# Performance work log

Hardware: AMD Instinct MI355X
Metric: run time of the kernel (lower is better)

The kernel has to match this reference:

```python
import jax, jax.numpy as jnp
import numpy as np

H_IMG = W_IMG = 1024
H_MAP = W_MAP = 64
SCALE = 16  # img // fmap, both axes
SCALES = [2, 2.5, 3, 3.5, 4, 5]
RATIOS = [0.5, 1.5, 2.0, 2.5, 3, 3.5, 4]
A = len(SCALES) * len(RATIOS)  # 42
POS_T, NEG_T = 0.5, 0.3


def _anchors_np():
    # generate_base_anchors + generate_anchor_boxes (down_h = down_w = SCALE)
    base = np.zeros((A, 4), np.float32)
    cy = cx = SCALE / 2.0
    i = 0
    for s in SCALES:
        for ar in RATIOS:
            h = SCALE * s * np.sqrt(ar)
            w = SCALE * s * np.sqrt(1.0 / ar)
            base[i] = [cy - h / 2.0, cx - w / 2.0, cy + h / 2.0, cx + w / 2.0]
            i += 1
    sy = np.arange(H_MAP) * SCALE
    sx = np.arange(W_MAP) * SCALE
    gx, gy = np.meshgrid(sx, sy)
    shifts = np.stack([gy.ravel(), gx.ravel(), gy.ravel(), gx.ravel()], axis=1)
    # order (H, W, A) -> matches conf.permute(0,2,3,1) flatten
    return (base[None, :, :] + shifts[:, None, :]).reshape(-1, 4).astype(np.float32)


def _conv(x, w, b):
    y = jax.lax.conv_general_dilated(x, w, (1, 1), 'SAME',
                                     dimension_numbers=('NCHW', 'OIHW', 'NCHW'))
    return y + b[None, :, None, None]


def setup_inputs() -> dict:
    key = jax.random.key(0)
    ks = jax.random.split(key, 10)
    B, N, C, Hm, Wm, HID = 8, 20, 256, 64, 64, 512
    feature_map = jax.random.normal(ks[0], (B, C, Hm, Wm), dtype=jnp.float32)
    # valid GT boxes in pixel xyxy-style (d0<d2, d1<d3), last 5 per image padded -1
    p0 = jax.random.uniform(ks[1], (B, N)) * 860.0
    p1 = jax.random.uniform(ks[2], (B, N)) * 860.0
    s0 = jax.random.uniform(ks[3], (B, N)) * 144.0 + 16.0
    s1 = jax.random.uniform(ks[4], (B, N)) * 144.0 + 16.0
    gt_bboxes = jnp.stack([p0, p1, p0 + s0, p1 + s1], axis=-1)
    gt_bboxes = gt_bboxes.at[:, 15:, :].set(-1.0)
    gt_classes = jax.random.randint(ks[5], (B, N), 0, 10)
    conv1_w = jax.random.normal(ks[6], (HID, C, 3, 3), dtype=jnp.float32) * 0.02
    conv1_b = jnp.zeros((HID,), jnp.float32)
    conf_w = jax.random.normal(ks[7], (A, HID, 1, 1), dtype=jnp.float32) * 0.02
    conf_b = jnp.zeros((A,), jnp.float32)
    reg_w = jax.random.normal(ks[8], (4 * A, HID, 1, 1), dtype=jnp.float32) * 0.02
    reg_b = jnp.zeros((4 * A,), jnp.float32)
    return {"feature_map": feature_map, "gt_bboxes": gt_bboxes, "gt_classes": gt_classes,
            "conv1_w": conv1_w, "conv1_b": conv1_b, "conf_w": conf_w, "conf_b": conf_b,
            "reg_w": reg_w, "reg_b": reg_b}


def reference(feature_map, gt_bboxes, gt_classes, conv1_w, conv1_b,
              conf_w, conf_b, reg_w, reg_b):
    anc = jnp.asarray(_anchors_np())           # [M,4]
    B = feature_map.shape[0]
    M = anc.shape[0]                           # H*W*A

    # project_bboxes p2a: divide by scale, keep -1 padding
    pad = gt_bboxes == -1.0
    g = jnp.where(pad, -1.0, gt_bboxes / float(SCALE))  # [B,N,4]
    valid = g[..., 0] >= 0                                # [B,N]
    g_safe = jnp.where(valid[..., None], g, jnp.array([0.0, 0.0, 1.0, 1.0]))

    # pairwise IoU [B,M,N] (vectorized get_iou_mat; invalid GT -> 0)
    tl = jnp.maximum(anc[None, :, None, :2], g_safe[:, None, :, :2])
    br = jnp.minimum(anc[None, :, None, 2:], g_safe[:, None, :, 2:])
    wh = jnp.clip(br - tl, 0.0)
    inter = wh[..., 0] * wh[..., 1]
    area_a = (anc[:, 2] - anc[:, 0]) * (anc[:, 3] - anc[:, 1])
    area_g = (g_safe[..., 2] - g_safe[..., 0]) * (g_safe[..., 3] - g_safe[..., 1])
    iou = inter / (area_a[None, :, None] + area_g[:, None, :] - inter)
    iou = jnp.where(valid[:, None, :], iou, 0.0)

    # positive assignment: per-GT argmax anchors + IoU > pos_thresh
    max_per_gt = iou.max(axis=1, keepdims=True)            # [B,1,N]
    pos_mask = ((iou == max_per_gt) & (max_per_gt > 0)) | (iou > POS_T)
    pos_any = pos_mask.any(axis=-1)                        # [B,M]
    a2g = jnp.argmax(iou, axis=2)                          # [B,M]
    max_per_anc = iou.max(axis=2)                          # [B,M]

    gt_for_anc = jnp.take_along_axis(g_safe, a2g[:, :, None], axis=1)  # [B,M,4]
    anc_b = jnp.broadcast_to(anc, (B, M, 4))
    gt_sel = jnp.where(pos_any[..., None], gt_for_anc, anc_b)  # safe for log

    # calc_gt_offsets (cxcywh encode), computed for all anchors, masked later
    a_c = (anc_b[..., :2] + anc_b[..., 2:]) * 0.5
    a_s = anc_b[..., 2:] - anc_b[..., :2]
    g_c = (gt_sel[..., :2] + gt_sel[..., 2:]) * 0.5
    g_s = gt_sel[..., 2:] - gt_sel[..., :2]
    off_gt = jnp.concatenate([(g_c - a_c) / a_s, jnp.log(g_s / a_s)], axis=-1)
    off_gt = off_gt.reshape(-1, 4)                          # [B*M,4]

    # ProposalModule head (dropout is a no-op in eval)
    x = jax.nn.relu(_conv(feature_map, conv1_w, conv1_b))
    conf = _conv(x, conf_w, conf_b)                         # [B,A,H,W]
    reg = _conv(x, reg_w, reg_b)                            # [B,4A,H,W]
    cflat = conf.transpose(0, 2, 3, 1).reshape(-1)          # [B*M]
    offp = reg.transpose(0, 2, 3, 1).reshape(-1, 4)         # [B*M,4]

    pf = pos_any.reshape(-1).astype(jnp.float32)
    P = pf.sum()

    # cls loss: BCE-with-logits, label 1 on positives, 0 on P sampled negatives
    cls_pos = (jax.nn.softplus(-cflat) * pf).sum() / P
    neg = max_per_anc.reshape(-1) < NEG_T
    scores = jax.random.uniform(jax.random.key(7), cflat.shape)
    scores = jnp.where(neg, scores, 2.0)
    ranks = jnp.argsort(jnp.argsort(scores))               # random sample = rank < P
    sel = (neg & (ranks < P)).astype(jnp.float32)
    cls_neg = (jax.nn.softplus(cflat) * sel).sum() / sel.sum()
    cls_loss = 0.5 * (cls_pos + cls_neg)

    d = offp - off_gt
    ad = jnp.abs(d)
    sl1 = jnp.where(ad < 1.0, 0.5 * ad * ad, ad - 0.5)
    reg_loss = (sl1 * pf[:, None]).sum() / (P * 4.0)

    return cls_loss + reg_loss
```

## Files before the change

kernel.cpp:

```cpp
#include <hip/hip_runtime.h>
#include <hip/hip_fp16.h>
#include <stdint.h>

constexpr int B_  = 8, HM = 64, WM = 64, A_ = 42, CIN = 256, HIDN = 512;
constexpr int M_  = HM * WM * A_;
constexpr int NA  = B_ * M_;
constexpr int HALF = NA / 2;
constexpr int KK  = CIN * 9;
constexpr float POS_T = 0.5f;

constexpr int WINY = 10, WINX = 10, WPIX = WINY * WINX;
constexpr int PERIMG = A_ * WPIX;
constexpr int WBLK = (PERIMG + 511) / 512;
constexpr int NMAXB = WBLK * B_;

constexpr int MAXPOS = 4096, MAXSEL = 4096;
constexpr int MAXPIX = 1024;
constexpr uint32_t VCAND = 16384u;
constexpr int NBIN = 128, CAP = 96;

constexpr int KCH = 288;

constexpr int NWIN = NMAXB;
constexpr int NRND = 168;
constexpr int NWCV = 72;
constexpr int NBLK_TF = NWIN + NRND + NWCV;

constexpr size_t OFF_CTRL  = 0;
constexpr size_t OFF_MAXGT = 256;
constexpr size_t OFF_BINSP = 1024;
constexpr size_t OFF_SLOT  = 9216;
constexpr size_t MS_END    = 140288;
constexpr size_t OFF_PLIST = 140288;
constexpr size_t OFF_POSL  = 144384;
constexpr size_t OFF_SELL  = 160768;
constexpr size_t OFF_CAND  = 177152;
constexpr size_t OFF_APATCH= 8689664;
constexpr size_t OFF_WF16  = 13408256;
constexpr size_t OFF_HFIN  = 15767552;


__device__ __forceinline__ unsigned short f2bf(float f) {
  uint32_t x = __float_as_uint(f);
  uint32_t r = x + 0x7FFFu + ((x >> 16) & 1u);
  return (unsigned short)(r >> 16);
}
__device__ __forceinline__ float bf2f(unsigned short h) {
  return __uint_as_float(((uint32_t)h) << 16);
}
__device__ __forceinline__ uint32_t f2h2(float a, float b) {
  return (uint32_t)__half_as_ushort(__float2half_rn(a)) |
         ((uint32_t)__half_as_ushort(__float2half_rn(b)) << 16);
}

typedef _Float16 h8v __attribute__((ext_vector_type(8)));
typedef float f4v __attribute__((ext_vector_type(4)));

__device__ __forceinline__ float iou_pair(float ay0, float ax0, float ay1, float ax1,
                                          float areaA, float g0, float g1, float g2, float g3,
                                          float areaG) {
#pragma clang fp contract(off)
  float ty = fmaxf(ay0, g0), tx = fmaxf(ax0, g1);
  float by = fminf(ay1, g2), bx = fminf(ax1, g3);
  float hy = by - ty; hy = fmaxf(hy, 0.f);
  float hx = bx - tx; hx = fmaxf(hx, 0.f);
  float inter = hy * hx;
  return inter / (areaA + areaG - inter);
}

__device__ __forceinline__ void anchor_box(const float* basef, int a, int y, int x,
                                           float& ay0, float& ax0, float& ay1, float& ax1,
                                           float& areaA) {
#pragma clang fp contract(off)
  double sy = 16.0 * (double)y, sx = 16.0 * (double)x;
  ay0 = (float)((double)basef[a * 4 + 0] + sy);
  ax0 = (float)((double)basef[a * 4 + 1] + sx);
  ay1 = (float)((double)basef[a * 4 + 2] + sy);
  ax1 = (float)((double)basef[a * 4 + 3] + sx);
  areaA = (ay1 - ay0) * (ax1 - ax0);
}

__device__ __forceinline__ void fill_base(float* sbase, int t) {
  if (t < 42) {
    const double SC[6] = {2.0, 2.5, 3.0, 3.5, 4.0, 5.0};
    const double RA[7] = {0.5, 1.5, 2.0, 2.5, 3.0, 3.5, 4.0};
    int si = t / 7, ri = t - si * 7;
    double h = 16.0 * SC[si] * sqrt(RA[ri]);
    double w = 16.0 * SC[si] * sqrt(1.0 / RA[ri]);
    sbase[t * 4 + 0] = (float)(8.0 - h / 2.0);
    sbase[t * 4 + 1] = (float)(8.0 - w / 2.0);
    sbase[t * 4 + 2] = (float)(8.0 + h / 2.0);
    sbase[t * 4 + 3] = (float)(8.0 + w / 2.0);
  }
}

__device__ __forceinline__ void fill_gt(const float* gt, int b, float* sg, float* sarea,
                                        unsigned* sval, int t) {
  if (t < 20) {
#pragma clang fp contract(off)
    float g4[4];
    for (int d = 0; d < 4; d++) {
      float v = gt[(b * 20 + t) * 4 + d];
      g4[d] = (v == -1.0f) ? -1.0f : v * 0.0625f;
    }
    unsigned valid = (g4[0] >= 0.0f) ? 1u : 0u;
    if (!valid) { g4[0] = 0.f; g4[1] = 0.f; g4[2] = 1.f; g4[3] = 1.f; }
    sg[t * 4 + 0] = g4[0]; sg[t * 4 + 1] = g4[1]; sg[t * 4 + 2] = g4[2]; sg[t * 4 + 3] = g4[3];
    sarea[t] = (g4[2] - g4[0]) * (g4[3] - g4[1]);
    sval[t] = valid;
  }
}

__device__ __forceinline__ void claim_pixel(char* ws, int pixg) {
  int* slotmap = (int*)(ws + OFF_SLOT);
  if (atomicCAS((unsigned*)&slotmap[pixg], 0u, 0xFFFFFFFFu) == 0u) {
    unsigned s = atomicAdd((unsigned*)(ws + OFF_CTRL) + 2, 1u);
    if (s < MAXPIX) { ((int*)(ws + OFF_PLIST))[s] = pixg; slotmap[pixg] = (int)s + 1; }
    else slotmap[pixg] = -1;
  }
}

__device__ __forceinline__ float softplusf(float x) {
  return fmaxf(x, 0.f) + log1pf(expf(-fabsf(x)));
}
__device__ __forceinline__ float sl1(float d) {
  float ad = fabsf(d);
  return ad < 1.f ? 0.5f * ad * ad : ad - 0.5f;
}

__device__ __forceinline__ void tf_round(uint32_t& x0, uint32_t& x1, int r) {
  x0 += x1; x1 = (x1 << r) | (x1 >> (32 - r)); x1 ^= x0;
}
__device__ __forceinline__ void threefry(uint32_t c0, uint32_t c1, uint32_t& o0, uint32_t& o1) {
  const uint32_t k0 = 0u, k1 = 7u;
  const uint32_t k2 = k0 ^ k1 ^ 0x1BD11BDAu;
  uint32_t x0 = c0 + k0, x1 = c1 + k1;
  tf_round(x0, x1, 13); tf_round(x0, x1, 15); tf_round(x0, x1, 26); tf_round(x0, x1, 6);
  x0 += k1; x1 += k2 + 1u;
  tf_round(x0, x1, 17); tf_round(x0, x1, 29); tf_round(x0, x1, 16); tf_round(x0, x1, 24);
  x0 += k2; x1 += k0 + 2u;
  tf_round(x0, x1, 13); tf_round(x0, x1, 15); tf_round(x0, x1, 26); tf_round(x0, x1, 6);
  x0 += k0; x1 += k1 + 3u;
  tf_round(x0, x1, 17); tf_round(x0, x1, 29); tf_round(x0, x1, 16); tf_round(x0, x1, 24);
  x0 += k1; x1 += k2 + 4u;
  tf_round(x0, x1, 13); tf_round(x0, x1, 15); tf_round(x0, x1, 26); tf_round(x0, x1, 6);
  x0 += k2; x1 += k0 + 5u;
  o0 = x0; o1 = x1;
}

__device__ __forceinline__ void emit_cand(char* ws, uint32_t v, uint32_t p) {
  if (v < VCAND) {
    unsigned bin = v >> 7;
    unsigned slot = atomicAdd((unsigned*)(ws + OFF_BINSP) + bin * 16, 1u);
    if (slot < (unsigned)CAP)
      ((uint2*)(ws + OFF_CAND))[bin * CAP + slot] = make_uint2(v, p);
  }
}

__global__ void __launch_bounds__(512) kTF(const float* __restrict__ gt,
                                           const float* __restrict__ w1, char* ws) {
  __shared__ float sbase[168], sg[80], sarea[20];
  __shared__ unsigned sval[20];
  __shared__ int smax[20];
  int t = threadIdx.x;
  if (blockIdx.x < NWIN) {
    int b = blockIdx.x / WBLK, blk = blockIdx.x - b * WBLK;
    fill_base(sbase, t);
    fill_gt(gt, b, sg, sarea, sval, t);
    if (t < 20) smax[t] = 0;
    __syncthreads();
    int idx = blk * 512 + t;
    bool ok = idx < PERIMG;
    float ay0 = 0.f, ax0 = 0.f, ay1 = 0.f, ax1 = 0.f, areaA = 1.f;
    if (ok) {
      int a = idx / WPIX, pp = idx - a * WPIX;
      int y = pp / WINX, x = pp - y * WINX;
      anchor_box(sbase, a, y, x, ay0, ax0, ay1, ax1, areaA);
    }
#pragma unroll
    for (int n = 0; n < 20; n++) {
      float io = 0.f;
      if (ok && sval[n]) io = iou_pair(ay0, ax0, ay1, ax1, areaA,
                                       sg[n * 4], sg[n * 4 + 1], sg[n * 4 + 2],
                                       sg[n * 4 + 3], sarea[n]);
#pragma unroll
      for (int off = 32; off >= 1; off >>= 1) io = fmaxf(io, __shfl_xor(io, off, 64));
      if ((t & 63) == 0 && io > 0.f) atomicMax(&smax[n], __float_as_int(io));
    }
    __syncthreads();
    if (t < 20 && smax[t] != 0)
      atomicMax((int*)(ws + OFF_MAXGT) + b * 20 + t, smax[t]);
  } else if (blockIdx.x < NWIN + NRND) {
    int p0 = ((int)blockIdx.x - NWIN) * 512 + t;
#pragma unroll
    for (int it = 0; it < 8; it++) {
      int p = p0 + it * (NRND * 512);
      uint32_t o0, o1; threefry((uint32_t)p, (uint32_t)(p + HALF), o0, o1);
      emit_cand(ws, o0 >> 9, (uint32_t)p);
      emit_cand(ws, o1 >> 9, (uint32_t)(p + HALF));
    }
  } else {
    int q0 = ((int)blockIdx.x - (NWIN + NRND)) * 512 + t;
#pragma unroll
    for (int it = 0; it < 8; it++) {
      int q = q0 + it * (NWCV * 512);
      float4 v = ((const float4*)w1)[q];
      uint2 o;
      o.x = f2h2(v.x, v.y);
      o.y = f2h2(v.z, v.w);
      ((uint2*)(ws + OFF_WF16))[q] = o;
    }
  }
}

__global__ void __launch_bounds__(512) kPos2(const float* __restrict__ gt, char* ws) {
  __shared__ float sbase[168], sg[80], sarea[20], smg[20];
  __shared__ unsigned sval[20];
  __shared__ unsigned scnt[128];
  __shared__ unsigned s_r, s_ucut;
  __shared__ int s_icut, s_cutbin, s_last;
  int b = blockIdx.y, t = threadIdx.x, lane = t & 63;
  unsigned* ctrl = (unsigned*)(ws + OFF_CTRL);
  fill_base(sbase, t);
  fill_gt(gt, b, sg, sarea, sval, t);
  if (t < 20) smg[t] = __int_as_float(((int*)(ws + OFF_MAXGT))[b * 20 + t]);
  __syncthreads();
  int idx = blockIdx.x * 512 + t;
  bool pos = false;
  unsigned packv = 0;
  int pixg = 0;
  if (idx < PERIMG) {
    int a = idx / WPIX, pp = idx - a * WPIX;
    int y = pp / WINX, x = pp - y * WINX;
    float ay0, ax0, ay1, ax1, areaA;
    anchor_box(sbase, a, y, x, ay0, ax0, ay1, ax1, areaA);
    float best = -1.f; int arg = 0;
#pragma unroll
    for (int n = 0; n < 20; n++) {
      float io = 0.f;
      if (sval[n]) io = iou_pair(ay0, ax0, ay1, ax1, areaA,
                                 sg[n * 4], sg[n * 4 + 1], sg[n * 4 + 2],
                                 sg[n * 4 + 3], sarea[n]);
      if (io > best) { best = io; arg = n; }
      float mg = smg[n];
      pos = pos || ((io == mg) && (mg > 0.f)) || (io > POS_T);
    }
    if (pos) {
      int pix = y * 64 + x;
      int i = b * M_ + pix * 42 + a;
      packv = (unsigned)i | ((unsigned)arg << 21);
      pixg = b * 4096 + pix;
    }
  }
  unsigned long long mask = __ballot(pos);
  if (mask) {
    int leader = (int)__ffsll(mask) - 1;
    unsigned base = 0;
    if (lane == leader) base = atomicAdd(&ctrl[0], (unsigned)__popcll(mask));
    base = (unsigned)__shfl((int)base, leader, 64);
    if (pos) {
      unsigned slot = base + (unsigned)__popcll(mask & ((1ull << lane) - 1ull));
      if (slot < MAXPOS) ((unsigned*)(ws + OFF_POSL))[slot] = packv;
      claim_pixel(ws, pixg);
    }
  }
  __syncthreads();
  if (t == 0) {
    unsigned r = __hip_atomic_fetch_add(&ctrl[11], 1u, __ATOMIC_RELAXED,
                                        __HIP_MEMORY_SCOPE_AGENT);
    s_last = (r == (unsigned)(WBLK * B_) - 1) ? 1 : 0;
  }
  __syncthreads();
  if (!s_last) return;
  const uint2* bucket = (const uint2*)(ws + OFF_CAND);
  unsigned P = min(__hip_atomic_load(&ctrl[0], __ATOMIC_RELAXED,
                                     __HIP_MEMORY_SCOPE_AGENT), (unsigned)MAXPOS);
  if (t < 128)
    scnt[t] = min(__hip_atomic_load((unsigned*)(ws + OFF_BINSP) + t * 16,
                                    __ATOMIC_RELAXED, __HIP_MEMORY_SCOPE_AGENT),
                  (unsigned)CAP);
  __syncthreads();
  if (t == 0) {
    unsigned cum = 0; int c = 0;
    for (; c < 128; c++) { if (cum + scnt[c] >= P) break; cum += scnt[c]; }
    if (c == 128) c = 127;
    s_cutbin = c; s_r = (P > cum) ? (P - cum) : 0u;
  }
  __syncthreads();
  int cutbin = s_cutbin;
  unsigned n = scnt[cutbin];
  unsigned r = s_r; if (r > n) r = n;
  if (r == 0) {
    if (t == 0) { s_ucut = 0; s_icut = -1; }
  } else if (t < (int)n) {
    uint2 mine = bucket[cutbin * CAP + t];
    unsigned rank = 0;
    for (unsigned j = 0; j < n; j++) {
      uint2 o = bucket[cutbin * CAP + j];
      if (o.x < mine.x || (o.x == mine.x && (int)o.y < (int)mine.y)) rank++;
    }
    if (rank == r - 1) { s_ucut = mine.x; s_icut = (int)mine.y; }
  }
  __syncthreads();
  unsigned ucut = s_ucut; int icut = s_icut;
  for (unsigned j = t; j < (unsigned)(NBIN * CAP); j += 512) {
    unsigned bin = j / CAP, k = j - bin * CAP;
    bool sel = false; uint2 cj = make_uint2(0u, 0u);
    if (k < scnt[bin]) {
      cj = bucket[j];
      sel = (cj.x < ucut) || (cj.x == ucut && (int)cj.y <= icut);
    }
    unsigned long long m2 = __ballot(sel);
    if (m2) {
      int leader = (int)__ffsll(m2) - 1;
      unsigned base = 0;
      if (lane == leader) base = atomicAdd(&ctrl[1], (unsigned)__popcll(m2));
      base = (unsigned)__shfl((int)base, leader, 64);
      if (sel) {
        unsigned slot = base + (unsigned)__popcll(m2 & ((1ull << lane) - 1ull));
        if (slot < MAXSEL) {
          ((int*)(ws + OFF_SELL))[slot] = (int)cj.y;
          int bb = (int)cj.y / M_; int m = (int)cj.y - bb * M_;
          claim_pixel(ws, bb * 4096 + m / 42);
        }
      }
    }
  }
}

__global__ void __launch_bounds__(256) kIm2col(const float* __restrict__ fm, char* ws) {
  unsigned* ctrl = (unsigned*)(ws + OFF_CTRL);
  int npix = min((int)ctrl[2], MAXPIX);
  int chunk = blockIdx.y;
  int u0 = chunk * 384;
  for (int blk = blockIdx.x; blk < npix; blk += gridDim.x) {
    int pixg = ((const int*)(ws + OFF_PLIST))[blk];
    int b = pixg >> 12, pix = pixg & 4095;
    int y = pix >> 6, x = pix & 63;
    uint32_t* Ap = (uint32_t*)(ws + OFF_APATCH) + (size_t)blk * (KK / 2);
    for (int u = u0 + threadIdx.x; u < u0 + 384; u += 256) {
      float v[2];
#pragma unroll
      for (int h = 0; h < 2; h++) {
        int k = 2 * u + h;
        int ic = k / 9, r = k - ic * 9;
        int dy = r / 3, dx = r - dy * 3;
        int yy = y + dy - 1, xx = x + dx - 1;
        float vv = 0.f;
        if (yy >= 0 && yy < 64 && xx >= 0 && xx < 64)
          vv = fm[(((size_t)b * CIN + ic) * 64 + yy) * 64 + xx];
        v[h] = vv;
      }
      Ap[u] = f2h2(v[0], v[1]);
    }
  }
}

__global__ void __launch_bounds__(512) kGemm(const float* __restrict__ b1, char* ws) {
  __shared__ float red[8][16][132];
  unsigned* ctrl = (unsigned*)(ws + OFF_CTRL);
  int npix = min((int)ctrl[2], MAXPIX);
  int strip = blockIdx.x, och = blockIdx.y;
  int px0 = strip * 16;
  if (px0 >= npix) return;
  int oc0 = och * 128;
  const _Float16* Ap = (const _Float16*)(ws + OFF_APATCH);
  const _Float16* Wf = (const _Float16*)(ws + OFF_WF16);
  int t = threadIdx.x, lane = t & 63, wv = t >> 6;
  int kq = lane >> 4;
  int kb = wv * KCH;
  const _Float16* Arow = Ap + (size_t)(px0 + (lane & 15)) * KK + kb + kq * 8;
  const _Float16* Wrow = Wf + (size_t)(oc0 + (lane & 15)) * KK + kb + kq * 8;
  f4v acc[8] = {};
#pragma unroll 3
  for (int s = 0; s < 9; s++) {
    h8v a = *(const h8v*)(Arow + s * 32);
#pragma unroll
    for (int o = 0; o < 8; o++) {
      h8v bfr = *(const h8v*)(Wrow + (size_t)o * 16 * KK + s * 32);
      acc[o] = __builtin_amdgcn_mfma_f32_16x16x32_f16(a, bfr, acc[o], 0, 0, 0);
    }
  }
#pragma unroll
  for (int o = 0; o < 8; o++) {
    int col = o * 16 + (lane & 15);
#pragma unroll
    for (int r = 0; r < 4; r++)
      red[wv][kq * 4 + r][col] = acc[o][r];
  }
  __syncthreads();
  int row = t >> 5, colg = t & 31;
  if (px0 + row < npix) {
    float s4[4];
#pragma unroll
    for (int j = 0; j < 4; j++) s4[j] = b1[oc0 + colg * 4 + j];
#pragma unroll
    for (int w = 0; w < 8; w++)
#pragma unroll
      for (int j = 0; j < 4; j++) s4[j] += red[w][row][colg * 4 + j];
#pragma unroll
    for (int j = 0; j < 4; j++) s4[j] = fmaxf(s4[j], 0.f);
    unsigned short* hf = (unsigned short*)(ws + OFF_HFIN);
    uint2 o2;
    o2.x = f2h2(s4[0], s4[1]);
    o2.y = f2h2(s4[2], s4[3]);
    *(uint2*)(hf + (size_t)(px0 + row) * HIDN + oc0 + colg * 4) = o2;
  }
}

__global__ void __launch_bounds__(256) kHead(const float* __restrict__ gt,
                                             const float* __restrict__ cw,
                                             const float* __restrict__ cb,
                                             const float* __restrict__ rw,
                                             const float* __restrict__ rb,
                                             char* ws, float* out) {
  __shared__ float sbase[168], sg[640];
  __shared__ float sacc[3];
  int t = threadIdx.x;
  fill_base(sbase, t);
  if (t < 160) {
#pragma clang fp contract(off)
    float g4[4];
    for (int d = 0; d < 4; d++) {
      float v = gt[t * 4 + d];
      g4[d] = (v == -1.0f) ? -1.0f : v * 0.0625f;
    }
    if (!(g4[0] >= 0.0f)) { g4[0] = 0.f; g4[1] = 0.f; g4[2] = 1.f; g4[3] = 1.f; }
    sg[t * 4 + 0] = g4[0]; sg[t * 4 + 1] = g4[1];
    sg[t * 4 + 2] = g4[2]; sg[t * 4 + 3] = g4[3];
  }
  if (t < 3) sacc[t] = 0.f;
  __syncthreads();
  unsigned* ctrl = (unsigned*)(ws + OFF_CTRL);
  float* accum = (float*)(ctrl + 16);
  int np = min((int)ctrl[0], MAXPOS);
  int ns = min((int)ctrl[1], MAXSEL);
  int nent = np + ns;
  const unsigned* posl = (const unsigned*)(ws + OFF_POSL);
  const int* sell = (const int*)(ws + OFF_SELL);
  const int* slotmap = (const int*)(ws + OFF_SLOT);
  const unsigned short* hfin = (const unsigned short*)(ws + OFF_HFIN);
  int lane = t & 63;
  int gwave = blockIdx.x * 4 + (t >> 6);
  int nwaves = gridDim.x * 4;
  for (int e = gwave; e < nent; e += nwaves) {
    bool isPos = e < np;
    int i, arg = 0;
    if (isPos) { unsigned pck = posl[e]; i = (int)(pck & 0x1FFFFFu); arg = (int)(pck >> 21); }
    else i = sell[e - np];
    int b = i / M_; int m = i - b * M_;
    int pix = m / 42; int a = m - pix * 42;
    int y = pix >> 6, x = pix & 63;
    int slot = slotmap[b * 4096 + pix] - 1;
    if (slot < 0 || slot >= MAXPIX) continue;
    float h[8];
    {
      h8v hv = *(const h8v*)(hfin + (size_t)slot * HIDN + lane * 8);
#pragma unroll
      for (int j = 0; j < 8; j++) h[j] = (float)hv[j];
    }
    const float* cwr = cw + (size_t)a * HIDN + lane * 8;
    float4 cA = *(const float4*)cwr;
    float4 cB = *(const float4*)(cwr + 4);
    float cp = h[0] * cA.x + h[1] * cA.y + h[2] * cA.z + h[3] * cA.w +
               h[4] * cB.x + h[5] * cB.y + h[6] * cB.z + h[7] * cB.w;
#pragma unroll
    for (int off = 32; off >= 1; off >>= 1) cp += __shfl_xor(cp, off, 64);
    float conf = cp + cb[a];
    if (isPos) {
      float rp[4];
#pragma unroll
      for (int d = 0; d < 4; d++) {
        const float* rwr = rw + (size_t)(a * 4 + d) * HIDN + lane * 8;
        float4 rA = *(const float4*)rwr;
        float4 rB = *(const float4*)(rwr + 4);
        float sd = h[0] * rA.x + h[1] * rA.y + h[2] * rA.z + h[3] * rA.w +
                   h[4] * rB.x + h[5] * rB.y + h[6] * rB.z + h[7] * rB.w;
#pragma unroll
        for (int off = 32; off >= 1; off >>= 1) sd += __shfl_xor(sd, off, 64);
        rp[d] = sd + rb[a * 4 + d];
      }
      if (lane == 0) {
#pragma clang fp contract(off)
        float ay0, ax0, ay1, ax1, areaA;
        anchor_box(sbase, a, y, x, ay0, ax0, ay1, ax1, areaA);
        const float* g = sg + (size_t)(b * 20 + arg) * 4;
        float acy = (ay0 + ay1) * 0.5f, acx = (ax0 + ax1) * 0.5f;
        float ah = ay1 - ay0, aw = ax1 - ax0;
        float gcy = (g[0] + g[2]) * 0.5f, gcx = (g[1] + g[3]) * 0.5f;
        float gh = g[2] - g[0], gw = g[3] - g[1];
        float t0 = (gcy - acy) / ah, t1 = (gcx - acx) / aw;
        float t2 = logf(gh / ah), t3 = logf(gw / aw);
        float sL = sl1(rp[0] - t0) + sl1(rp[1] - t1) + sl1(rp[2] - t2) + sl1(rp[3] - t3);
        atomicAdd(&sacc[2], sL);
        atomicAdd(&sacc[0], softplusf(-conf));
      }
    } else {
      if (lane == 0) atomicAdd(&sacc[1], softplusf(conf));
    }
  }
  __syncthreads();
  if (t == 0) {
    if (sacc[0] != 0.f) atomicAdd(&accum[0], sacc[0]);
    if (sacc[1] != 0.f) atomicAdd(&accum[1], sacc[1]);
    if (sacc[2] != 0.f) atomicAdd(&accum[2], sacc[2]);
    asm volatile("s_waitcnt vmcnt(0)" ::: "memory");
    unsigned done = __hip_atomic_fetch_add(&ctrl[10], 1u, __ATOMIC_RELAXED,
                                           __HIP_MEMORY_SCOPE_AGENT);
    if (done == gridDim.x - 1) {
      float a0 = __hip_atomic_load(&accum[0], __ATOMIC_RELAXED, __HIP_MEMORY_SCOPE_AGENT);
      float a1 = __hip_atomic_load(&accum[1], __ATOMIC_RELAXED, __HIP_MEMORY_SCOPE_AGENT);
      float a2 = __hip_atomic_load(&accum[2], __ATOMIC_RELAXED, __HIP_MEMORY_SCOPE_AGENT);
      float P = (float)min((int)ctrl[0], MAXPOS);
      float S = (float)min((int)ctrl[1], MAXSEL);
      float cls = 0.5f * (a0 / P + a1 / S);
      out[0] = cls + a2 / (P * 4.0f);
    }
  }
}

extern "C" void kernel_launch(void* const* d_in, const int* in_sizes, int n_in,
                              void* d_out, int out_size, void* d_ws, size_t ws_size,
                              hipStream_t stream) {
  const float* fm = (const float*)d_in[0];
  const float* gt = (const float*)d_in[1];
  const float* w1 = (const float*)d_in[3];
  const float* b1 = (const float*)d_in[4];
  const float* cw = (const float*)d_in[5];
  const float* cb = (const float*)d_in[6];
  const float* rw = (const float*)d_in[7];
  const float* rb = (const float*)d_in[8];
  char* ws = (char*)d_ws;
  float* out = (float*)d_out;

  hipMemsetAsync(ws, 0, MS_END, stream);
  kTF<<<NBLK_TF, 512, 0, stream>>>(gt, w1, ws);
  kPos2<<<dim3(WBLK, B_), 512, 0, stream>>>(gt, ws);
  kIm2col<<<dim3(128, 3), 256, 0, stream>>>(fm, ws);
  kGemm<<<dim3(MAXPIX / 16, 4), 512, 0, stream>>>(b1, ws);
  kHead<<<256, 256, 0, stream>>>(gt, cw, cb, rw, rb, ws, out);
}
```

Baseline: 162.6 us.

## Move weight fp16 cast into im2col launch and widen GEMM pixel tile

The conv1 weight fp32-to-fp16 conversion moves out of the first kernel and into extra blocks of the im2col launch, so it overlaps with patch gathering and stays off the early critical path. The GEMM now gives each block 32 pixels, with 2 pixel groups and 4 K chunks instead of 8 K chunks over 16 pixels. This halves the block count and reuses each loaded weight fragment across twice as many pixels, at the cost of a longer per-wave K loop. The head grid doubles to 512 blocks, and an atomic load of the bin counters becomes a plain load.

New measurement: 183.5 us. +12.8%, slower.

```diff
diff --git a/kernel.cpp b/kernel.cpp
--- a/kernel.cpp
+++ b/kernel.cpp
@@ -19,12 +19,13 @@
 constexpr uint32_t VCAND = 16384u;
 constexpr int NBIN = 128, CAP = 96;
 
-constexpr int KCH = 288;
-
 constexpr int NWIN = NMAXB;
 constexpr int NRND = 168;
-constexpr int NWCV = 72;
-constexpr int NBLK_TF = NWIN + NRND + NWCV;
+constexpr int NBLK_TF = NWIN + NRND;
+
+constexpr int NI2C = 128, NWCV = 72;
+
+constexpr int KCH4 = 576;
 
 constexpr size_t OFF_CTRL  = 0;
 constexpr size_t OFF_MAXGT = 256;
@@ -40,14 +41,6 @@
 constexpr size_t OFF_HFIN  = 15767552;
 
 
-__device__ __forceinline__ unsigned short f2bf(float f) {
-  uint32_t x = __float_as_uint(f);
-  uint32_t r = x + 0x7FFFu + ((x >> 16) & 1u);
-  return (unsigned short)(r >> 16);
-}
-__device__ __forceinline__ float bf2f(unsigned short h) {
-  return __uint_as_float(((uint32_t)h) << 16);
-}
 __device__ __forceinline__ uint32_t f2h2(float a, float b) {
   return (uint32_t)__half_as_ushort(__float2half_rn(a)) |
          ((uint32_t)__half_as_ushort(__float2half_rn(b)) << 16);
@@ -157,8 +150,7 @@
   }
 }
 
-__global__ void __launch_bounds__(512) kTF(const float* __restrict__ gt,
-                                           const float* __restrict__ w1, char* ws) {
+__global__ void __launch_bounds__(512) kTF(const float* __restrict__ gt, char* ws) {
   __shared__ float sbase[168], sg[80], sarea[20];
   __shared__ unsigned sval[20];
   __shared__ int smax[20];
@@ -190,7 +182,7 @@
     __syncthreads();
     if (t < 20 && smax[t] != 0)
       atomicMax((int*)(ws + OFF_MAXGT) + b * 20 + t, smax[t]);
-  } else if (blockIdx.x < NWIN + NRND) {
+  } else {
     int p0 = ((int)blockIdx.x - NWIN) * 512 + t;
 #pragma unroll
     for (int it = 0; it < 8; it++) {
@@ -198,17 +190,6 @@
       uint32_t o0, o1; threefry((uint32_t)p, (uint32_t)(p + HALF), o0, o1);
       emit_cand(ws, o0 >> 9, (uint32_t)p);
       emit_cand(ws, o1 >> 9, (uint32_t)(p + HALF));
-    }
-  } else {
-    int q0 = ((int)blockIdx.x - (NWIN + NRND)) * 512 + t;
-#pragma unroll
-    for (int it = 0; it < 8; it++) {
-      int q = q0 + it * (NWCV * 512);
-      float4 v = ((const float4*)w1)[q];
-      uint2 o;
-      o.x = f2h2(v.x, v.y);
-      o.y = f2h2(v.z, v.w);
-      ((uint2*)(ws + OFF_WF16))[q] = o;
     }
   }
 }
@@ -276,9 +257,7 @@
   unsigned P = min(__hip_atomic_load(&ctrl[0], __ATOMIC_RELAXED,
                                      __HIP_MEMORY_SCOPE_AGENT), (unsigned)MAXPOS);
   if (t < 128)
-    scnt[t] = min(__hip_atomic_load((unsigned*)(ws + OFF_BINSP) + t * 16,
-                                    __ATOMIC_RELAXED, __HIP_MEMORY_SCOPE_AGENT),
-                  (unsigned)CAP);
+    scnt[t] = min(((const unsigned*)(ws + OFF_BINSP))[t * 16], (unsigned)CAP);
   __syncthreads();
   if (t == 0) {
     unsigned cum = 0; int c = 0;
@@ -328,12 +307,27 @@
   }
 }
 
-__global__ void __launch_bounds__(256) kIm2col(const float* __restrict__ fm, char* ws) {
+__global__ void __launch_bounds__(256) kIm2col(const float* __restrict__ fm,
+                                               const float* __restrict__ w1, char* ws) {
+  if (blockIdx.x >= NI2C) {
+    if (blockIdx.y != 0) return;
+    int q0 = ((int)blockIdx.x - NI2C) * 256 + threadIdx.x;
+#pragma unroll
+    for (int it = 0; it < 16; it++) {
+      int q = q0 + it * (NWCV * 256);
+      float4 v = ((const float4*)w1)[q];
+      uint2 o;
+      o.x = f2h2(v.x, v.y);
+      o.y = f2h2(v.z, v.w);
+      ((uint2*)(ws + OFF_WF16))[q] = o;
+    }
+    return;
+  }
   unsigned* ctrl = (unsigned*)(ws + OFF_CTRL);
   int npix = min((int)ctrl[2], MAXPIX);
   int chunk = blockIdx.y;
   int u0 = chunk * 384;
-  for (int blk = blockIdx.x; blk < npix; blk += gridDim.x) {
+  for (int blk = blockIdx.x; blk < npix; blk += NI2C) {
     int pixg = ((const int*)(ws + OFF_PLIST))[blk];
     int b = pixg >> 12, pix = pixg & 4095;
     int y = pix >> 6, x = pix & 63;
@@ -357,23 +351,24 @@
 }
 
 __global__ void __launch_bounds__(512) kGemm(const float* __restrict__ b1, char* ws) {
-  __shared__ float red[8][16][132];
+  __shared__ float red[4][2][16][132];
   unsigned* ctrl = (unsigned*)(ws + OFF_CTRL);
   int npix = min((int)ctrl[2], MAXPIX);
   int strip = blockIdx.x, och = blockIdx.y;
-  int px0 = strip * 16;
+  int px0 = strip * 32;
   if (px0 >= npix) return;
   int oc0 = och * 128;
   const _Float16* Ap = (const _Float16*)(ws + OFF_APATCH);
   const _Float16* Wf = (const _Float16*)(ws + OFF_WF16);
   int t = threadIdx.x, lane = t & 63, wv = t >> 6;
+  int pxg = wv & 1, kc = wv >> 1;
   int kq = lane >> 4;
-  int kb = wv * KCH;
-  const _Float16* Arow = Ap + (size_t)(px0 + (lane & 15)) * KK + kb + kq * 8;
+  int kb = kc * KCH4;
+  const _Float16* Arow = Ap + (size_t)(px0 + pxg * 16 + (lane & 15)) * KK + kb + kq * 8;
   const _Float16* Wrow = Wf + (size_t)(oc0 + (lane & 15)) * KK + kb + kq * 8;
   f4v acc[8] = {};
 #pragma unroll 3
-  for (int s = 0; s < 9; s++) {
+  for (int s = 0; s < 18; s++) {
     h8v a = *(const h8v*)(Arow + s * 32);
 #pragma unroll
     for (int o = 0; o < 8; o++) {
@@ -386,25 +381,29 @@
     int col = o * 16 + (lane & 15);
 #pragma unroll
     for (int r = 0; r < 4; r++)
-      red[wv][kq * 4 + r][col] = acc[o][r];
-  }
-  __syncthreads();
-  int row = t >> 5, colg = t & 31;
-  if (px0 + row < npix) {
-    float s4[4];
-#pragma unroll
-    for (int j = 0; j < 4; j++) s4[j] = b1[oc0 + colg * 4 + j];
-#pragma unroll
-    for (int w = 0; w < 8; w++)
-#pragma unroll
-      for (int j = 0; j < 4; j++) s4[j] += red[w][row][colg * 4 + j];
-#pragma unroll
-    for (int j = 0; j < 4; j++) s4[j] = fmaxf(s4[j], 0.f);
-    unsigned short* hf = (unsigned short*)(ws + OFF_HFIN);
-    uint2 o2;
-    o2.x = f2h2(s4[0], s4[1]);
-    o2.y = f2h2(s4[2], s4[3]);
-    *(uint2*)(hf + (size_t)(px0 + row) * HIDN + oc0 + colg * 4) = o2;
+      red[kc][pxg][kq * 4 + r][col] = acc[o][r];
+  }
+  __syncthreads();
+#pragma unroll
+  for (int i = 0; i < 2; i++) {
+    int slot = t + i * 512;
+    int pxl = slot >> 5, colg = slot & 31;
+    if (px0 + pxl < npix) {
+      float s4[4];
+#pragma unroll
+      for (int j = 0; j < 4; j++) s4[j] = b1[oc0 + colg * 4 + j];
+#pragma unroll
+      for (int k2 = 0; k2 < 4; k2++)
+#pragma unroll
+        for (int j = 0; j < 4; j++) s4[j] += red[k2][pxl >> 4][pxl & 15][colg * 4 + j];
+#pragma unroll
+      for (int j = 0; j < 4; j++) s4[j] = fmaxf(s4[j], 0.f);
+      unsigned short* hf = (unsigned short*)(ws + OFF_HFIN);
+      uint2 o2;
+      o2.x = f2h2(s4[0], s4[1]);
+      o2.y = f2h2(s4[2], s4[3]);
+      *(uint2*)(hf + (size_t)(px0 + pxl) * HIDN + oc0 + colg * 4) = o2;
+    }
   }
 }
 
@@ -534,9 +533,9 @@
   float* out = (float*)d_out;
 
   hipMemsetAsync(ws, 0, MS_END, stream);
-  kTF<<<NBLK_TF, 512, 0, stream>>>(gt, w1, ws);
+  kTF<<<NBLK_TF, 512, 0, stream>>>(gt, ws);
   kPos2<<<dim3(WBLK, B_), 512, 0, stream>>>(gt, ws);
-  kIm2col<<<dim3(128, 3), 256, 0, stream>>>(fm, ws);
-  kGemm<<<dim3(MAXPIX / 16, 4), 512, 0, stream>>>(b1, ws);
-  kHead<<<256, 256, 0, stream>>>(gt, cw, cb, rw, rb, ws, out);
-}
+  kIm2col<<<dim3(NI2C + NWCV, 3), 256, 0, stream>>>(fm, w1, ws);
+  kGemm<<<dim3(MAXPIX / 32, 4), 512, 0, stream>>>(b1, ws);
+  kHead<<<512, 256, 0, stream>>>(gt, cw, cb, rw, rb, ws, out);
+}
```
